# Optimization experiments

Hardware: AMD Instinct MI355X
Metric: run time of the kernel (lower is better)

## Reference

```python
import jax, jax.numpy as jnp
import numpy as np

D_K = 64  # hardcoded in the original module
NEG_INF = -1.0e9


def setup_inputs() -> dict:
    key = jax.random.key(0)
    kq, kk, kv = jax.random.split(key, 3)
    B, H, S, D = 2, 16, 2048, D_K
    Q = jax.random.normal(kq, (B, H, S, D), dtype=jnp.float32)
    K = jax.random.normal(kk, (B, H, S, D), dtype=jnp.float32)
    V = jax.random.normal(kv, (B, H, S, D), dtype=jnp.float32)
    # causal mask: True means masked out (matches masked_fill_ semantics)
    causal = jnp.triu(jnp.ones((S, S), dtype=jnp.bool_), k=1)
    attn_mask = jnp.broadcast_to(causal, (B, H, S, S))
    return {"Q": Q, "K": K, "V": V, "attn_mask": attn_mask}


def reference(Q, K, V, attn_mask):
    # scores = Q @ (K^T / sqrt(d_k))
    scale = 1.0 / np.sqrt(D_K).astype(np.float32)
    scores = jnp.einsum("bhqd,bhkd->bhqk", Q, K * scale)  # [B,H,S,S]
    scores = jnp.where(attn_mask, NEG_INF, scores)
    attn_scores = jax.nn.softmax(scores, axis=-1)
    context = jnp.einsum("bhqk,bhkd->bhqd", attn_scores, V)
    return (context, attn_scores)
```

## Files before the change

### kernel.cpp

```cpp
#include <hip/hip_runtime.h>
#include <stdint.h>

typedef float  f32x4  __attribute__((ext_vector_type(4)));
typedef short  s16x4  __attribute__((ext_vector_type(4)));
typedef short  s16x8  __attribute__((ext_vector_type(8)));

#define S_LEN 2048
#define D_K   64
#define NBH   32
#define VT_STRIDE (S_LEN + 32)
#define MFMA  __builtin_amdgcn_mfma_f32_16x16x32_bf16

__device__ __forceinline__ short f2bf(float f) {
    uint32_t u = __builtin_bit_cast(uint32_t, f);
    u += 0x7fffu + ((u >> 16) & 1u);
    return (short)(u >> 16);
}
__device__ __forceinline__ s16x4 cvt4(float4 f) {
    s16x4 r; r[0] = f2bf(f.x); r[1] = f2bf(f.y); r[2] = f2bf(f.z); r[3] = f2bf(f.w);
    return r;
}
__device__ __forceinline__ s16x8 cat(s16x4 a, s16x4 b) {
    return __builtin_shufflevector(a, b, 0, 1, 2, 3, 4, 5, 6, 7);
}
__device__ __forceinline__ void nt_store4(float* p, f32x4 v) {
    __builtin_nontemporal_store(v, (f32x4*)p);
}

__global__ __launch_bounds__(256) void preconv(
    const float* __restrict__ K, const float* __restrict__ V,
    short* __restrict__ Kb, short* __restrict__ VT)
{
    const int bh  = blockIdx.x >> 6;
    const int seg = blockIdx.x & 63;
    const int tid = threadIdx.x;
    const float* Ks = K + ((size_t)bh * S_LEN + seg * 32) * D_K;
    const float* Vs = V + ((size_t)bh * S_LEN + seg * 32) * D_K;
    short* Kd  = Kb + ((size_t)bh * S_LEN + seg * 32) * D_K;
    short* VTd = VT + (size_t)bh * D_K * VT_STRIDE + seg * 32;

    for (int i = tid; i < 512; i += 256) {
        const int r = i >> 4, ci = i & 15;
        float4 f = *(const float4*)(Ks + r * D_K + (ci << 2));
        const int j = ((ci & 3) << 1) + ((ci >> 2) & 1) + ((ci >> 3) << 3);
        *(s16x4*)(Kd + r * D_K + (j << 2)) = cvt4(f);
    }
    for (int i = tid; i < 512; i += 256) {
        const int r = i & 31, c = (i >> 5) << 2;
        float4 f = *(const float4*)(Vs + r * D_K + c);
        const int rp = (((r & 15) >> 2) << 3) + (((r >> 4) & 1) << 2) + (r & 3);
        VTd[(size_t)(c + 0) * VT_STRIDE + rp] = f2bf(f.x);
        VTd[(size_t)(c + 1) * VT_STRIDE + rp] = f2bf(f.y);
        VTd[(size_t)(c + 2) * VT_STRIDE + rp] = f2bf(f.z);
        VTd[(size_t)(c + 3) * VT_STRIDE + rp] = f2bf(f.w);
    }
}

#define PSTR 517
#define CHUNK 16
__global__ __launch_bounds__(256) void attn_pair(
    const float* __restrict__ Q, const short* __restrict__ Kb,
    const short* __restrict__ VT, float* __restrict__ outC,
    float* __restrict__ outS)
{
    __shared__ float pstg[32 * PSTR];
    __shared__ float lbuf[4][32];

    const int tid = threadIdx.x, lane = tid & 63, wv = tid >> 6;
    const int xcd = blockIdx.x & 7;
    const int idx = blockIdx.x >> 3;
    const int bh  = (xcd << 2) + (idx >> 6);
    const int j   = 63 - (idx & 63);
    const int q0  = j << 5;
    const int l15 = lane & 15;
    const int g   = lane >> 4;
    const int d0  = g << 2;
    const int qa  = q0 + l15;

    const short* Kbh = Kb + (size_t)bh * S_LEN * D_K;
    const short* VTh = VT + (size_t)bh * D_K * VT_STRIDE;
    float* outSb = outS + (size_t)bh * S_LEN * S_LEN;
    float* outCb = outC + (size_t)bh * S_LEN * D_K;

    s16x8 qf0a, qf1a, qf0b, qf1b;
    {
        const float4* qp = (const float4*)(Q + ((size_t)bh * S_LEN + qa) * D_K);
        qf0a = cat(cvt4(qp[g]),     cvt4(qp[g + 4]));
        qf1a = cat(cvt4(qp[g + 8]), cvt4(qp[g + 12]));
        const float4* qp2 = (const float4*)(Q + ((size_t)bh * S_LEN + qa + 16) * D_K);
        qf0b = cat(cvt4(qp2[g]),     cvt4(qp2[g + 4]));
        qf1b = cat(cvt4(qp2[g + 8]), cvt4(qp2[g + 12]));
    }

    const int ntiles = j + 1;
    const float scale = 0.125f;

    float la = 0.f, lb = 0.f;
    {
        auto LD = [&](s16x8& r0, s16x8& r1, s16x8& r2, s16x8& r3, int t) {
            const short* p = Kbh + (((size_t)t << 5) + l15) * D_K + (g << 3);
            r0 = *(const s16x8*)(p);
            r1 = *(const s16x8*)(p + 32);
            r2 = *(const s16x8*)(p + 16 * D_K);
            r3 = *(const s16x8*)(p + 16 * D_K + 32);
        };
        auto SUM = [&](s16x8 r0, s16x8 r1, s16x8 r2, s16x8 r3, int T) {
            f32x4 a0 = {0.f,0.f,0.f,0.f}, a1 = a0, b0 = a0, b1 = a0;
            a0 = MFMA(r0, qf0a, a0, 0,0,0);
            a0 = MFMA(r1, qf1a, a0, 0,0,0);
            a1 = MFMA(r2, qf0a, a1, 0,0,0);
            a1 = MFMA(r3, qf1a, a1, 0,0,0);
            b0 = MFMA(r0, qf0b, b0, 0,0,0);
            b0 = MFMA(r1, qf1b, b0, 0,0,0);
            b1 = MFMA(r2, qf0b, b1, 0,0,0);
            b1 = MFMA(r3, qf1b, b1, 0,0,0);
            if (T < j) {
                #pragma unroll
                for (int r = 0; r < 4; ++r) {
                    la += __expf(a0[r] * scale) + __expf(a1[r] * scale);
                    lb += __expf(b0[r] * scale) + __expf(b1[r] * scale);
                }
            } else {
                const int kb0 = (T << 5) + d0;
                #pragma unroll
                for (int r = 0; r < 4; ++r) {
                    const bool c = (kb0 + r) <= qa;
                    if (c) la += __expf(a0[r] * scale);
                    lb += __expf(b0[r] * scale);
                    if (c) lb += __expf(b1[r] * scale);
                }
            }
        };
        s16x8 A0,A1,A2,A3, B0,B1,B2,B3, C0,C1,C2,C3;
        int t = wv;
        if (t < ntiles) {
            LD(A0,A1,A2,A3, t);
            if (t + 4 < ntiles) LD(B0,B1,B2,B3, t + 4);
            if (t + 8 < ntiles) LD(C0,C1,C2,C3, t + 8);
            for (;;) {
                SUM(A0,A1,A2,A3, t);
                t += 4;
                if (t >= ntiles) break;
                if (t + 8 < ntiles) LD(A0,A1,A2,A3, t + 8);
                SUM(B0,B1,B2,B3, t);
                t += 4;
                if (t >= ntiles) break;
                if (t + 8 < ntiles) LD(B0,B1,B2,B3, t + 8);
                SUM(C0,C1,C2,C3, t);
                t += 4;
                if (t >= ntiles) break;
                if (t + 8 < ntiles) LD(C0,C1,C2,C3, t + 8);
            }
        }
    }
    la += __shfl_xor(la, 16); la += __shfl_xor(la, 32);
    lb += __shfl_xor(lb, 16); lb += __shfl_xor(lb, 32);
    if (lane < 16) { lbuf[wv][l15] = la; lbuf[wv][16 + l15] = lb; }
    __syncthreads();
    const float rinva = 1.f / (lbuf[0][l15] + lbuf[1][l15] + lbuf[2][l15] + lbuf[3][l15]);
    const float rinvb = 1.f / (lbuf[0][16 + l15] + lbuf[1][16 + l15]
                             + lbuf[2][16 + l15] + lbuf[3][16 + l15]);

    f32x4 cxa0 = {0.f,0.f,0.f,0.f}, cxa1 = cxa0, cxa2 = cxa0, cxa3 = cxa0;
    f32x4 cxb0 = cxa0, cxb1 = cxa0, cxb2 = cxa0, cxb3 = cxa0;
    {
        s16x8 k0[4], v0[4], k1[4], v1[4];

        auto LDK = [&](s16x8* kk, s16x8* vv, int t) {
            const short* kp = Kbh + (((size_t)t << 5) + l15) * D_K + (g << 3);
            kk[0] = *(const s16x8*)(kp);
            kk[1] = *(const s16x8*)(kp + 32);
            kk[2] = *(const s16x8*)(kp + 16 * D_K);
            kk[3] = *(const s16x8*)(kp + 16 * D_K + 32);
            const short* vp = VTh + (size_t)l15 * VT_STRIDE + (t << 5) + (g << 3);
            vv[0] = *(const s16x8*)(vp);
            vv[1] = *(const s16x8*)(vp + 16 * VT_STRIDE);
            vv[2] = *(const s16x8*)(vp + 32 * VT_STRIDE);
            vv[3] = *(const s16x8*)(vp + 48 * VT_STRIDE);
        };
        auto CMPS = [&](const s16x8* kk, const s16x8* vv, int T, int tt) {
            f32x4 a0 = {0.f,0.f,0.f,0.f}, a1 = a0, b0 = a0, b1 = a0;
            a0 = MFMA(kk[0], qf0a, a0, 0,0,0);
            a0 = MFMA(kk[1], qf1a, a0, 0,0,0);
            a1 = MFMA(kk[2], qf0a, a1, 0,0,0);
            a1 = MFMA(kk[3], qf1a, a1, 0,0,0);
            b0 = MFMA(kk[0], qf0b, b0, 0,0,0);
            b0 = MFMA(kk[1], qf1b, b0, 0,0,0);
            b1 = MFMA(kk[2], qf0b, b1, 0,0,0);
            b1 = MFMA(kk[3], qf1b, b1, 0,0,0);
            f32x4 pa0, pa1, pb0, pb1;
            s16x8 pfa, pfb;
            if (T < j) {
                #pragma unroll
                for (int r = 0; r < 4; ++r) {
                    float ea0 = __expf(a0[r] * scale) * rinva;
                    float ea1 = __expf(a1[r] * scale) * rinva;
                    float eb0 = __expf(b0[r] * scale) * rinvb;
                    float eb1 = __expf(b1[r] * scale) * rinvb;
                    pa0[r] = ea0; pa1[r] = ea1; pb0[r] = eb0; pb1[r] = eb1;
                    pfa[r] = f2bf(ea0); pfa[4 + r] = f2bf(ea1);
                    pfb[r] = f2bf(eb0); pfb[4 + r] = f2bf(eb1);
                }
            } else {
                const int kb0 = (T << 5) + d0;
                #pragma unroll
                for (int r = 0; r < 4; ++r) {
                    const bool c = (kb0 + r) <= qa;
                    float ea0 = c ? __expf(a0[r] * scale) * rinva : 0.f;
                    float eb0 = __expf(b0[r] * scale) * rinvb;
                    float eb1 = c ? __expf(b1[r] * scale) * rinvb : 0.f;
                    pa0[r] = ea0; pa1[r] = 0.f; pb0[r] = eb0; pb1[r] = eb1;
                    pfa[r] = f2bf(ea0); pfa[4 + r] = 0;
                    pfb[r] = f2bf(eb0); pfb[4 + r] = f2bf(eb1);
                }
            }
            float* sa = &pstg[l15 * PSTR + (tt << 5) + d0];
            float* sb = &pstg[(16 + l15) * PSTR + (tt << 5) + d0];
            *(f32x4*)(sa)      = pa0;
            *(f32x4*)(sa + 16) = pa1;
            *(f32x4*)(sb)      = pb0;
            *(f32x4*)(sb + 16) = pb1;
            cxa0 = MFMA(pfa, vv[0], cxa0, 0,0,0);
            cxa1 = MFMA(pfa, vv[1], cxa1, 0,0,0);
            cxa2 = MFMA(pfa, vv[2], cxa2, 0,0,0);
            cxa3 = MFMA(pfa, vv[3], cxa3, 0,0,0);
            cxb0 = MFMA(pfb, vv[0], cxb0, 0,0,0);
            cxb1 = MFMA(pfb, vv[1], cxb1, 0,0,0);
            cxb2 = MFMA(pfb, vv[2], cxb2, 0,0,0);
            cxb3 = MFMA(pfb, vv[3], cxb3, 0,0,0);
        };

        if (wv < ntiles)     LDK(k0, v0, wv);
        if (wv + 4 < ntiles) LDK(k1, v1, wv + 4);

        for (int cb = 0; cb < ntiles; cb += CHUNK) {
            for (int sb = cb; sb < cb + CHUNK && sb < ntiles; sb += 8) {
                const int tA = sb + wv, tB = sb + wv + 4;
                if (tA < ntiles) CMPS(k0, v0, tA, tA - cb);
                const int nA = sb + 8 + wv;
                if (nA < ntiles) LDK(k0, v0, nA);
                if (tB < ntiles) CMPS(k1, v1, tB, tB - cb);
                const int nB = sb + 12 + wv;
                if (nB < ntiles) LDK(k1, v1, nB);
            }
            asm volatile("s_waitcnt lgkmcnt(0)" ::: "memory");
            __builtin_amdgcn_s_barrier();
            const int rem = ntiles - cb;
            const int W = ((rem < CHUNK) ? rem : CHUNK) << 5;
            const size_t gb = (size_t)q0 * S_LEN + ((size_t)cb << 5);
            #pragma unroll
            for (int rr = 0; rr < 8; ++rr) {
                const int row = (rr << 2) + wv;
                for (int c = lane << 2; c < W; c += 256)
                    nt_store4(outSb + gb + (size_t)row * S_LEN + c,
                              *(const f32x4*)&pstg[row * PSTR + c]);
            }
            asm volatile("s_waitcnt lgkmcnt(0)" ::: "memory");
            __builtin_amdgcn_s_barrier();
        }
    }

    const int kz = ntiles << 5;
    const f32x4 z = {0.f,0.f,0.f,0.f};
    {
        const int c0 = tid << 2;
        for (int r = 0; r < 32; ++r) {
            float* rowp = outSb + (size_t)(q0 + r) * S_LEN;
            for (int k = kz + c0; k < S_LEN; k += 1024)
                nt_store4(rowp + k, z);
        }
    }

    __syncthreads();
    {
        float* cb2 = pstg;
        #pragma unroll
        for (int r = 0; r < 4; ++r) {
            cb2[wv * 2112 + (d0 + r) * 66 +  0 + l15] = cxa0[r];
            cb2[wv * 2112 + (d0 + r) * 66 + 16 + l15] = cxa1[r];
            cb2[wv * 2112 + (d0 + r) * 66 + 32 + l15] = cxa2[r];
            cb2[wv * 2112 + (d0 + r) * 66 + 48 + l15] = cxa3[r];
            cb2[wv * 2112 + (16 + d0 + r) * 66 +  0 + l15] = cxb0[r];
            cb2[wv * 2112 + (16 + d0 + r) * 66 + 16 + l15] = cxb1[r];
            cb2[wv * 2112 + (16 + d0 + r) * 66 + 32 + l15] = cxb2[r];
            cb2[wv * 2112 + (16 + d0 + r) * 66 + 48 + l15] = cxb3[r];
        }
        __syncthreads();
        const int dbase = (tid & 15) << 2;
        for (int rr = tid >> 4; rr < 32; rr += 16) {
            f32x4 acc = *(const f32x4*)&cb2[0 * 2112 + rr * 66 + dbase];
            #pragma unroll
            for (int w = 1; w < 4; ++w) {
                f32x4 p = *(const f32x4*)&cb2[w * 2112 + rr * 66 + dbase];
                acc[0] += p[0]; acc[1] += p[1]; acc[2] += p[2]; acc[3] += p[3];
            }
            *(f32x4*)(outCb + (size_t)(q0 + rr) * D_K + dbase) = acc;
        }
    }
}

#define KSTRIDE 68
#define VSTRIDE 36
__global__ __launch_bounds__(256) void attn_causal_fb(
    const float* __restrict__ Q, const float* __restrict__ K,
    const float* __restrict__ V, float* __restrict__ outC,
    float* __restrict__ outS)
{
    __shared__ short Klds[32 * KSTRIDE];
    __shared__ short Vlds[64 * VSTRIDE];
    const int bh = blockIdx.x >> 5, q0 = (blockIdx.x & 31) << 6;
    const int tid = threadIdx.x, lane = tid & 63, wv = tid >> 6;
    const int q0w = q0 + (wv << 4), l15 = lane & 15, d0 = (lane >> 4) << 2;
    const int qg = q0w + l15, qhi = q0w + 15;
    const float* Kb = K + (size_t)bh * S_LEN * D_K;
    const float* Vb = V + (size_t)bh * S_LEN * D_K;
    float* outSb = outS + (size_t)bh * S_LEN * S_LEN;
    float* outCb = outC + (size_t)bh * S_LEN * D_K;
    s16x8 qf0, qf1;
    {
        const float4* qp = (const float4*)(Q + ((size_t)bh * S_LEN + qg) * D_K);
        qf0 = cat(cvt4(qp[d0 >> 2]), cvt4(qp[(d0 + 16) >> 2]));
        qf1 = cat(cvt4(qp[(d0 + 32) >> 2]), cvt4(qp[(d0 + 48) >> 2]));
    }
    const int npairs = (q0 >> 5) + 2;
    const float scale = 0.125f;
    float lsum = 0.f;
    for (int p = 0; p < npairs; ++p) {
        const int k0 = p << 5;
        for (int i = tid; i < 512; i += 256) {
            const int r = i >> 4, c = (i & 15) << 2;
            float4 f = *(const float4*)(Kb + (size_t)(k0 + r) * D_K + c);
            *(s16x4*)&Klds[r * KSTRIDE + c] = cvt4(f);
        }
        __syncthreads();
        if (k0 <= qhi) {
            #pragma unroll
            for (int s = 0; s < 2; ++s) {
                const short* kp = &Klds[(16 * s + l15) * KSTRIDE + d0];
                s16x8 a0 = cat(*(const s16x4*)kp, *(const s16x4*)(kp + 16));
                s16x8 a1 = cat(*(const s16x4*)(kp + 32), *(const s16x4*)(kp + 48));
                f32x4 c1 = {0.f,0.f,0.f,0.f};
                c1 = MFMA(a0, qf0, c1, 0,0,0);
                c1 = MFMA(a1, qf1, c1, 0,0,0);
                const int kbase = k0 + 16 * s + d0;
                #pragma unroll
                for (int r = 0; r < 4; ++r)
                    if (kbase + r <= qg) lsum += __expf(c1[r] * scale);
            }
        }
        __syncthreads();
    }
    lsum += __shfl_xor(lsum, 16);
    lsum += __shfl_xor(lsum, 32);
    const float rinv = 1.f / lsum;
    f32x4 ctx[4] = {{0,0,0,0},{0,0,0,0},{0,0,0,0},{0,0,0,0}};
    for (int p = 0; p < npairs; ++p) {
        const int k0 = p << 5;
        for (int i = tid; i < 512; i += 256) {
            const int r = i >> 4, c = (i & 15) << 2;
            float4 f = *(const float4*)(Kb + (size_t)(k0 + r) * D_K + c);
            *(s16x4*)&Klds[r * KSTRIDE + c] = cvt4(f);
            float4 gg = *(const float4*)(Vb + (size_t)(k0 + r) * D_K + c);
            Vlds[(c + 0) * VSTRIDE + r] = f2bf(gg.x);
            Vlds[(c + 1) * VSTRIDE + r] = f2bf(gg.y);
            Vlds[(c + 2) * VSTRIDE + r] = f2bf(gg.z);
            Vlds[(c + 3) * VSTRIDE + r] = f2bf(gg.w);
        }
        __syncthreads();
        if (k0 <= qhi) {
            s16x8 pf;
            #pragma unroll
            for (int s = 0; s < 2; ++s) {
                const short* kp = &Klds[(16 * s + l15) * KSTRIDE + d0];
                s16x8 a0 = cat(*(const s16x4*)kp, *(const s16x4*)(kp + 16));
                s16x8 a1 = cat(*(const s16x4*)(kp + 32), *(const s16x4*)(kp + 48));
                f32x4 c1 = {0.f,0.f,0.f,0.f};
                c1 = MFMA(a0, qf0, c1, 0,0,0);
                c1 = MFMA(a1, qf1, c1, 0,0,0);
                const int kbase = k0 + 16 * s + d0;
                f32x4 pw;
                #pragma unroll
                for (int r = 0; r < 4; ++r) {
                    float pe = (kbase + r <= qg) ? __expf(c1[r] * scale) * rinv : 0.f;
                    pw[r] = pe;
                    pf[4 * s + r] = f2bf(pe);
                }
                *(f32x4*)(outSb + (size_t)qg * S_LEN + kbase) = pw;
            }
            #pragma unroll
            for (int db = 0; db < 4; ++db) {
                const short* vp = &Vlds[(db * 16 + l15) * VSTRIDE + d0];
                s16x8 b = cat(*(const s16x4*)vp, *(const s16x4*)(vp + 16));
                ctx[db] = MFMA(pf, b, ctx[db], 0,0,0);
            }
        }
        __syncthreads();
    }
    #pragma unroll
    for (int db = 0; db < 4; ++db)
        #pragma unroll
        for (int r = 0; r < 4; ++r)
            outCb[(size_t)(q0w + d0 + r) * D_K + db * 16 + l15] = ctx[db][r];
    const int kz = ((qhi >> 5) + 1) << 5;
    const f32x4 z = {0.f,0.f,0.f,0.f};
    for (int r = 0; r < 16; ++r) {
        float* rowp = outSb + (size_t)(q0w + r) * S_LEN;
        for (int k = kz + (lane << 2); k < S_LEN; k += 256)
            *(f32x4*)(rowp + k) = z;
    }
}

extern "C" void kernel_launch(void* const* d_in, const int* in_sizes, int n_in,
                              void* d_out, int out_size, void* d_ws, size_t ws_size,
                              hipStream_t stream) {
    const float* Q = (const float*)d_in[0];
    const float* K = (const float*)d_in[1];
    const float* V = (const float*)d_in[2];
    float* outC = (float*)d_out;
    float* outS = (float*)d_out + (size_t)NBH * S_LEN * D_K;

    const size_t kb_elems = (size_t)NBH * S_LEN * D_K;
    const size_t vt_elems = (size_t)NBH * D_K * VT_STRIDE;
    const size_t need = (kb_elems + vt_elems) * sizeof(short);

    if (ws_size >= need) {
        short* Kb = (short*)d_ws;
        short* VT = Kb + kb_elems;
        preconv<<<dim3(NBH * 64), dim3(256), 0, stream>>>(K, V, Kb, VT);
        attn_pair<<<dim3(2048), dim3(256), 0, stream>>>(Q, Kb, VT, outC, outS);
    } else {
        attn_causal_fb<<<dim3(1024), dim3(256), 0, stream>>>(Q, K, V, outC, outS);
    }
}
```

Baseline: 157.1 us.

## Fuse softmax passes by stashing unnormalized bf16 probabilities in LDS

Replaces the two-pass scheme with a single pass. Before, QK^T and exp were computed once for the row sums and again for the probabilities. Now each exp is computed once, accumulated into the row sums, and stored unnormalized as bf16 in a full-row LDS stash, while the context accumulates unnormalized. At the end the context is scaled by the reciprocal sums, and full score rows, including the masked zero tail, are written from the stash in one pass. This halves the QK MFMAs and K loads, but the large LDS stash (~128KB) limits occupancy to one block per CU, and the stored scores are now rounded to bf16 before normalization.

```diff
diff --git a/kernel.cpp b/kernel.cpp
--- a/kernel.cpp
+++ b/kernel.cpp
@@ -15,6 +15,10 @@
     uint32_t u = __builtin_bit_cast(uint32_t, f);
     u += 0x7fffu + ((u >> 16) & 1u);
     return (short)(u >> 16);
+}
+__device__ __forceinline__ float bf2f(short s) {
+    uint32_t u = ((uint32_t)(uint16_t)s) << 16;
+    return __builtin_bit_cast(float, u);
 }
 __device__ __forceinline__ s16x4 cvt4(float4 f) {
     s16x4 r; r[0] = f2bf(f.x); r[1] = f2bf(f.y); r[2] = f2bf(f.z); r[3] = f2bf(f.w);
@@ -42,8 +46,8 @@
     for (int i = tid; i < 512; i += 256) {
         const int r = i >> 4, ci = i & 15;
         float4 f = *(const float4*)(Ks + r * D_K + (ci << 2));
-        const int j = ((ci & 3) << 1) + ((ci >> 2) & 1) + ((ci >> 3) << 3);
-        *(s16x4*)(Kd + r * D_K + (j << 2)) = cvt4(f);
+        const int jj = ((ci & 3) << 1) + ((ci >> 2) & 1) + ((ci >> 3) << 3);
+        *(s16x4*)(Kd + r * D_K + (jj << 2)) = cvt4(f);
     }
     for (int i = tid; i < 512; i += 256) {
         const int r = i & 31, c = (i >> 5) << 2;
@@ -56,14 +60,13 @@
     }
 }
 
-#define PSTR 517
-#define CHUNK 16
-__global__ __launch_bounds__(256) void attn_pair(
+#define SSTR 2056
+__global__ __launch_bounds__(256) void attn_sp(
     const float* __restrict__ Q, const short* __restrict__ Kb,
     const short* __restrict__ VT, float* __restrict__ outC,
     float* __restrict__ outS)
 {
-    __shared__ float pstg[32 * PSTR];
+    __shared__ __align__(16) char smem[32 * SSTR * 2];
     __shared__ float lbuf[4][32];
 
     const int tid = threadIdx.x, lane = tid & 63, wv = tid >> 6;
@@ -81,6 +84,7 @@
     const short* VTh = VT + (size_t)bh * D_K * VT_STRIDE;
     float* outSb = outS + (size_t)bh * S_LEN * S_LEN;
     float* outCb = outC + (size_t)bh * S_LEN * D_K;
+    short* sstash = (short*)smem;
 
     s16x8 qf0a, qf1a, qf0b, qf1b;
     {
@@ -96,73 +100,9 @@
     const float scale = 0.125f;
 
     float la = 0.f, lb = 0.f;
-    {
-        auto LD = [&](s16x8& r0, s16x8& r1, s16x8& r2, s16x8& r3, int t) {
-            const short* p = Kbh + (((size_t)t << 5) + l15) * D_K + (g << 3);
-            r0 = *(const s16x8*)(p);
-            r1 = *(const s16x8*)(p + 32);
-            r2 = *(const s16x8*)(p + 16 * D_K);
-            r3 = *(const s16x8*)(p + 16 * D_K + 32);
-        };
-        auto SUM = [&](s16x8 r0, s16x8 r1, s16x8 r2, s16x8 r3, int T) {
-            f32x4 a0 = {0.f,0.f,0.f,0.f}, a1 = a0, b0 = a0, b1 = a0;
-            a0 = MFMA(r0, qf0a, a0, 0,0,0);
-            a0 = MFMA(r1, qf1a, a0, 0,0,0);
-            a1 = MFMA(r2, qf0a, a1, 0,0,0);
-            a1 = MFMA(r3, qf1a, a1, 0,0,0);
-            b0 = MFMA(r0, qf0b, b0, 0,0,0);
-            b0 = MFMA(r1, qf1b, b0, 0,0,0);
-            b1 = MFMA(r2, qf0b, b1, 0,0,0);
-            b1 = MFMA(r3, qf1b, b1, 0,0,0);
-            if (T < j) {
-                #pragma unroll
-                for (int r = 0; r < 4; ++r) {
-                    la += __expf(a0[r] * scale) + __expf(a1[r] * scale);
-                    lb += __expf(b0[r] * scale) + __expf(b1[r] * scale);
-                }
-            } else {
-                const int kb0 = (T << 5) + d0;
-                #pragma unroll
-                for (int r = 0; r < 4; ++r) {
-                    const bool c = (kb0 + r) <= qa;
-                    if (c) la += __expf(a0[r] * scale);
-                    lb += __expf(b0[r] * scale);
-                    if (c) lb += __expf(b1[r] * scale);
-                }
-            }
-        };
-        s16x8 A0,A1,A2,A3, B0,B1,B2,B3, C0,C1,C2,C3;
-        int t = wv;
-        if (t < ntiles) {
-            LD(A0,A1,A2,A3, t);
-            if (t + 4 < ntiles) LD(B0,B1,B2,B3, t + 4);
-            if (t + 8 < ntiles) LD(C0,C1,C2,C3, t + 8);
-            for (;;) {
-                SUM(A0,A1,A2,A3, t);
-                t += 4;
-                if (t >= ntiles) break;
-                if (t + 8 < ntiles) LD(A0,A1,A2,A3, t + 8);
-                SUM(B0,B1,B2,B3, t);
-                t += 4;
-                if (t >= ntiles) break;
-                if (t + 8 < ntiles) LD(B0,B1,B2,B3, t + 8);
-                SUM(C0,C1,C2,C3, t);
-                t += 4;
-                if (t >= ntiles) break;
-                if (t + 8 < ntiles) LD(C0,C1,C2,C3, t + 8);
-            }
-        }
-    }
-    la += __shfl_xor(la, 16); la += __shfl_xor(la, 32);
-    lb += __shfl_xor(lb, 16); lb += __shfl_xor(lb, 32);
-    if (lane < 16) { lbuf[wv][l15] = la; lbuf[wv][16 + l15] = lb; }
-    __syncthreads();
-    const float rinva = 1.f / (lbuf[0][l15] + lbuf[1][l15] + lbuf[2][l15] + lbuf[3][l15]);
-    const float rinvb = 1.f / (lbuf[0][16 + l15] + lbuf[1][16 + l15]
-                             + lbuf[2][16 + l15] + lbuf[3][16 + l15]);
-
-    f32x4 cxa0 = {0.f,0.f,0.f,0.f}, cxa1 = cxa0, cxa2 = cxa0, cxa3 = cxa0;
-    f32x4 cxb0 = cxa0, cxb1 = cxa0, cxb2 = cxa0, cxb3 = cxa0;
+    f32x4 z4 = {0.f,0.f,0.f,0.f};
+    f32x4 cxa0 = z4, cxa1 = z4, cxa2 = z4, cxa3 = z4;
+    f32x4 cxb0 = z4, cxb1 = z4, cxb2 = z4, cxb3 = z4;
     {
         s16x8 k0[4], v0[4], k1[4], v1[4];
 
@@ -178,48 +118,44 @@
             vv[2] = *(const s16x8*)(vp + 32 * VT_STRIDE);
             vv[3] = *(const s16x8*)(vp + 48 * VT_STRIDE);
         };
-        auto CMPS = [&](const s16x8* kk, const s16x8* vv, int T, int tt) {
-            f32x4 a0 = {0.f,0.f,0.f,0.f}, a1 = a0, b0 = a0, b1 = a0;
-            a0 = MFMA(kk[0], qf0a, a0, 0,0,0);
-            a0 = MFMA(kk[1], qf1a, a0, 0,0,0);
-            a1 = MFMA(kk[2], qf0a, a1, 0,0,0);
-            a1 = MFMA(kk[3], qf1a, a1, 0,0,0);
-            b0 = MFMA(kk[0], qf0b, b0, 0,0,0);
-            b0 = MFMA(kk[1], qf1b, b0, 0,0,0);
-            b1 = MFMA(kk[2], qf0b, b1, 0,0,0);
-            b1 = MFMA(kk[3], qf1b, b1, 0,0,0);
-            f32x4 pa0, pa1, pb0, pb1;
+        auto CMPS = [&](const s16x8* kk, const s16x8* vv, int T) {
+            f32x4 sa0 = z4, sa1 = z4, sb0 = z4, sb1 = z4;
+            sa0 = MFMA(kk[0], qf0a, sa0, 0,0,0);
+            sa0 = MFMA(kk[1], qf1a, sa0, 0,0,0);
+            sa1 = MFMA(kk[2], qf0a, sa1, 0,0,0);
+            sa1 = MFMA(kk[3], qf1a, sa1, 0,0,0);
+            sb0 = MFMA(kk[0], qf0b, sb0, 0,0,0);
+            sb0 = MFMA(kk[1], qf1b, sb0, 0,0,0);
+            sb1 = MFMA(kk[2], qf0b, sb1, 0,0,0);
+            sb1 = MFMA(kk[3], qf1b, sb1, 0,0,0);
             s16x8 pfa, pfb;
             if (T < j) {
                 #pragma unroll
                 for (int r = 0; r < 4; ++r) {
-                    float ea0 = __expf(a0[r] * scale) * rinva;
-                    float ea1 = __expf(a1[r] * scale) * rinva;
-                    float eb0 = __expf(b0[r] * scale) * rinvb;
-                    float eb1 = __expf(b1[r] * scale) * rinvb;
-                    pa0[r] = ea0; pa1[r] = ea1; pb0[r] = eb0; pb1[r] = eb1;
-                    pfa[r] = f2bf(ea0); pfa[4 + r] = f2bf(ea1);
-                    pfb[r] = f2bf(eb0); pfb[4 + r] = f2bf(eb1);
+                    float e;
+                    e = __expf(sa0[r] * scale); la += e; pfa[r]   = f2bf(e);
+                    e = __expf(sa1[r] * scale); la += e; pfa[4+r] = f2bf(e);
+                    e = __expf(sb0[r] * scale); lb += e; pfb[r]   = f2bf(e);
+                    e = __expf(sb1[r] * scale); lb += e; pfb[4+r] = f2bf(e);
                 }
             } else {
-                const int kb0 = (T << 5) + d0;
                 #pragma unroll
                 for (int r = 0; r < 4; ++r) {
-                    const bool c = (kb0 + r) <= qa;
-                    float ea0 = c ? __expf(a0[r] * scale) * rinva : 0.f;
-                    float eb0 = __expf(b0[r] * scale) * rinvb;
-                    float eb1 = c ? __expf(b1[r] * scale) * rinvb : 0.f;
-                    pa0[r] = ea0; pa1[r] = 0.f; pb0[r] = eb0; pb1[r] = eb1;
-                    pfa[r] = f2bf(ea0); pfa[4 + r] = 0;
-                    pfb[r] = f2bf(eb0); pfb[4 + r] = f2bf(eb1);
-                }
-            }
-            float* sa = &pstg[l15 * PSTR + (tt << 5) + d0];
-            float* sb = &pstg[(16 + l15) * PSTR + (tt << 5) + d0];
-            *(f32x4*)(sa)      = pa0;
-            *(f32x4*)(sa + 16) = pa1;
-            *(f32x4*)(sb)      = pb0;
-            *(f32x4*)(sb + 16) = pb1;
+                    const bool c = (d0 + r) <= l15;
+                    float e;
+                    e = c ? __expf(sa0[r] * scale) : 0.f; la += e; pfa[r] = f2bf(e);
+                    pfa[4+r] = 0;
+                    e = __expf(sb0[r] * scale);           lb += e; pfb[r] = f2bf(e);
+                    e = c ? __expf(sb1[r] * scale) : 0.f; lb += e; pfb[4+r] = f2bf(e);
+                }
+            }
+            const int cbase = (T << 5) + d0;
+            short* sA = &sstash[l15 * SSTR + cbase];
+            *(s16x4*)(sA)      = __builtin_shufflevector(pfa, pfa, 0, 1, 2, 3);
+            *(s16x4*)(sA + 16) = __builtin_shufflevector(pfa, pfa, 4, 5, 6, 7);
+            short* sB = &sstash[(16 + l15) * SSTR + cbase];
+            *(s16x4*)(sB)      = __builtin_shufflevector(pfb, pfb, 0, 1, 2, 3);
+            *(s16x4*)(sB + 16) = __builtin_shufflevector(pfb, pfb, 4, 5, 6, 7);
             cxa0 = MFMA(pfa, vv[0], cxa0, 0,0,0);
             cxa1 = MFMA(pfa, vv[1], cxa1, 0,0,0);
             cxa2 = MFMA(pfa, vv[2], cxa2, 0,0,0);
@@ -230,68 +166,87 @@
             cxb3 = MFMA(pfb, vv[3], cxb3, 0,0,0);
         };
 
-        if (wv < ntiles)     LDK(k0, v0, wv);
-        if (wv + 4 < ntiles) LDK(k1, v1, wv + 4);
-
-        for (int cb = 0; cb < ntiles; cb += CHUNK) {
-            for (int sb = cb; sb < cb + CHUNK && sb < ntiles; sb += 8) {
-                const int tA = sb + wv, tB = sb + wv + 4;
-                if (tA < ntiles) CMPS(k0, v0, tA, tA - cb);
-                const int nA = sb + 8 + wv;
-                if (nA < ntiles) LDK(k0, v0, nA);
-                if (tB < ntiles) CMPS(k1, v1, tB, tB - cb);
-                const int nB = sb + 12 + wv;
-                if (nB < ntiles) LDK(k1, v1, nB);
-            }
-            asm volatile("s_waitcnt lgkmcnt(0)" ::: "memory");
-            __builtin_amdgcn_s_barrier();
-            const int rem = ntiles - cb;
-            const int W = ((rem < CHUNK) ? rem : CHUNK) << 5;
-            const size_t gb = (size_t)q0 * S_LEN + ((size_t)cb << 5);
-            #pragma unroll
-            for (int rr = 0; rr < 8; ++rr) {
-                const int row = (rr << 2) + wv;
-                for (int c = lane << 2; c < W; c += 256)
-                    nt_store4(outSb + gb + (size_t)row * S_LEN + c,
-                              *(const f32x4*)&pstg[row * PSTR + c]);
-            }
-            asm volatile("s_waitcnt lgkmcnt(0)" ::: "memory");
-            __builtin_amdgcn_s_barrier();
-        }
+        int t = wv;
+        if (t < ntiles) {
+            LDK(k0, v0, t);
+            while (t + 4 < ntiles) {
+                LDK(k1, v1, t + 4);
+                CMPS(k0, v0, t);
+                t += 4;
+                if (t + 4 < ntiles) {
+                    LDK(k0, v0, t + 4);
+                    CMPS(k1, v1, t);
+                    t += 4;
+                } else {
+                    CMPS(k1, v1, t);
+                    t += 4;
+                    break;
+                }
+            }
+            if (t < ntiles) CMPS(k0, v0, t);
+        }
+    }
+    la += __shfl_xor(la, 16); la += __shfl_xor(la, 32);
+    lb += __shfl_xor(lb, 16); lb += __shfl_xor(lb, 32);
+    if (lane < 16) { lbuf[wv][l15] = la; lbuf[wv][16 + l15] = lb; }
+    __syncthreads();
+    #pragma unroll
+    for (int r = 0; r < 4; ++r) {
+        const float ra = 1.f / (lbuf[0][d0 + r] + lbuf[1][d0 + r]
+                              + lbuf[2][d0 + r] + lbuf[3][d0 + r]);
+        const float rb = 1.f / (lbuf[0][16 + d0 + r] + lbuf[1][16 + d0 + r]
+                              + lbuf[2][16 + d0 + r] + lbuf[3][16 + d0 + r]);
+        cxa0[r] *= ra; cxa1[r] *= ra; cxa2[r] *= ra; cxa3[r] *= ra;
+        cxb0[r] *= rb; cxb1[r] *= rb; cxb2[r] *= rb; cxb3[r] *= rb;
     }
 
     const int kz = ntiles << 5;
-    const f32x4 z = {0.f,0.f,0.f,0.f};
-    {
-        const int c0 = tid << 2;
-        for (int r = 0; r < 32; ++r) {
-            float* rowp = outSb + (size_t)(q0 + r) * S_LEN;
-            for (int k = kz + c0; k < S_LEN; k += 1024)
-                nt_store4(rowp + k, z);
+    {
+        #pragma unroll
+        for (int rr8 = 0; rr8 < 8; ++rr8) {
+            const int row = (wv << 3) + rr8;
+            const float rinv_r = 1.f /
+                (lbuf[0][row] + lbuf[1][row] + lbuf[2][row] + lbuf[3][row]);
+            float* rowp = outSb + (size_t)(q0 + row) * S_LEN;
+            const short* srow = &sstash[row * SSTR];
+            for (int c = lane << 2; c < S_LEN; c += 256) {
+                f32x4 v;
+                if (c < kz) {
+                    s16x4 sv = *(const s16x4*)(srow + c);
+                    v[0] = bf2f(sv[0]) * rinv_r;
+                    v[1] = bf2f(sv[1]) * rinv_r;
+                    v[2] = bf2f(sv[2]) * rinv_r;
+                    v[3] = bf2f(sv[3]) * rinv_r;
+                } else {
+                    v[0] = 0.f; v[1] = 0.f; v[2] = 0.f; v[3] = 0.f;
+                }
+                nt_store4(rowp + c, v);
+            }
         }
     }
 
     __syncthreads();
     {
-        float* cb2 = pstg;
+        float* cb2 = (float*)smem;
+        const int base = wv * 2080;
         #pragma unroll
         for (int r = 0; r < 4; ++r) {
-            cb2[wv * 2112 + (d0 + r) * 66 +  0 + l15] = cxa0[r];
-            cb2[wv * 2112 + (d0 + r) * 66 + 16 + l15] = cxa1[r];
-            cb2[wv * 2112 + (d0 + r) * 66 + 32 + l15] = cxa2[r];
-            cb2[wv * 2112 + (d0 + r) * 66 + 48 + l15] = cxa3[r];
-            cb2[wv * 2112 + (16 + d0 + r) * 66 +  0 + l15] = cxb0[r];
-            cb2[wv * 2112 + (16 + d0 + r) * 66 + 16 + l15] = cxb1[r];
-            cb2[wv * 2112 + (16 + d0 + r) * 66 + 32 + l15] = cxb2[r];
-            cb2[wv * 2112 + (16 + d0 + r) * 66 + 48 + l15] = cxb3[r];
+            cb2[base + (d0 + r) * 65 +  0 + l15] = cxa0[r];
+            cb2[base + (d0 + r) * 65 + 16 + l15] = cxa1[r];
+            cb2[base + (d0 + r) * 65 + 32 + l15] = cxa2[r];
+            cb2[base + (d0 + r) * 65 + 48 + l15] = cxa3[r];
+            cb2[base + (16 + d0 + r) * 65 +  0 + l15] = cxb0[r];
+            cb2[base + (16 + d0 + r) * 65 + 16 + l15] = cxb1[r];
+            cb2[base + (16 + d0 + r) * 65 + 32 + l15] = cxb2[r];
+            cb2[base + (16 + d0 + r) * 65 + 48 + l15] = cxb3[r];
         }
         __syncthreads();
         const int dbase = (tid & 15) << 2;
         for (int rr = tid >> 4; rr < 32; rr += 16) {
-            f32x4 acc = *(const f32x4*)&cb2[0 * 2112 + rr * 66 + dbase];
+            f32x4 acc = *(const f32x4*)&cb2[0 * 2080 + rr * 65 + dbase];
             #pragma unroll
             for (int w = 1; w < 4; ++w) {
-                f32x4 p = *(const f32x4*)&cb2[w * 2112 + rr * 66 + dbase];
+                f32x4 p = *(const f32x4*)&cb2[w * 2080 + rr * 65 + dbase];
                 acc[0] += p[0]; acc[1] += p[1]; acc[2] += p[2]; acc[3] += p[3];
             }
             *(f32x4*)(outCb + (size_t)(q0 + rr) * D_K + dbase) = acc;
@@ -427,7 +382,7 @@
         short* Kb = (short*)d_ws;
         short* VT = Kb + kb_elems;
         preconv<<<dim3(NBH * 64), dim3(256), 0, stream>>>(K, V, Kb, VT);
-        attn_pair<<<dim3(2048), dim3(256), 0, stream>>>(Q, Kb, VT, outC, outS);
+        attn_sp<<<dim3(2048), dim3(256), 0, stream>>>(Q, Kb, VT, outC, outS);
     } else {
         attn_causal_fb<<<dim3(1024), dim3(256), 0, stream>>>(Q, K, V, outC, outS);
     }
```

Result: faster. 147.1 us (-6.4%).
